# Performance work log

Measured on AMD Instinct MI355X. Metric: run time of the kernel, lower is better.

The kernel has to match this reference:

```python
import jax, jax.numpy as jnp
import numpy as np

B, N, C = 16, 4096, 512
PW, PH = 64, 64  # N = PW * PH
POOL = 2         # attention_pool_scale
D_SCALE = 1.0 / float(np.sqrt(C))


def setup_inputs() -> dict:
    key = jax.random.key(0)
    ks = jax.random.split(key, 4)
    w_std = 1.0 / float(np.sqrt(C))
    return {
        "x": jax.random.normal(ks[0], (B, N, C), dtype=jnp.float32),
        "Wq": jax.random.normal(ks[1], (C, C), dtype=jnp.float32) * w_std,
        "bq": jnp.zeros((C,), dtype=jnp.float32),
        "Wk": jax.random.normal(ks[2], (C, C), dtype=jnp.float32) * w_std,
        "bk": jnp.zeros((C,), dtype=jnp.float32),
        "Wv": jax.random.normal(ks[3], (C, C), dtype=jnp.float32) * w_std,
        "bv": jnp.zeros((C,), dtype=jnp.float32),
    }


def _to_spatial(t):
    # [B, N, C] -> [B, C, PW, PH]
    return t.transpose(0, 2, 1).reshape(t.shape[0], C, PW, PH)


def reference(x, Wq, bq, Wk, bk, Wv, bv):
    # Linear (torch convention y = x @ W^T + b) + sigmoid activation
    def proj(W, b):
        return jax.nn.sigmoid(jnp.einsum('bnc,dc->bnd', x, W) + b)

    Q = _to_spatial(proj(Wq, bq))  # [B, C, PW, PH]
    K = _to_spatial(proj(Wk, bk))
    V = _to_spatial(proj(Wv, bv))

    # avg_pool2d with kernel (POOL, 1): pool over PW axis
    q = Q.reshape(B, C, PW // POOL, POOL, PH).mean(axis=3)  # [B, C, PW/2, PH]
    k = K.reshape(B, C, PW // POOL, POOL, PH).mean(axis=3)

    # Qk = softmax(scale * Q @ k^T): [B, C, PW, PW/2]
    Qk = jax.nn.softmax(D_SCALE * jnp.einsum('bcik,bcjk->bcij', Q, k), axis=-1)
    # Kq = softmax(scale * q @ K^T): [B, C, PW/2, PW]
    Kq = jax.nn.softmax(D_SCALE * jnp.einsum('bcik,bcjk->bcij', q, K), axis=-1)
    # Kqv = Kq @ V: [B, C, PW/2, PH]
    Kqv = jnp.einsum('bcij,bcjk->bcik', Kq, V)
    # out = Qk @ Kqv: [B, C, PW, PH]
    out = jnp.einsum('bcij,bcjk->bcik', Qk, Kqv)

    # spatial -> sequence: [B, C, PW*PH] -> [B, N, C]
    return out.reshape(B, C, N).transpose(0, 2, 1)
```

## Files before the change

### kernel.cpp

```cpp
#include <hip/hip_runtime.h>
#include <hip/hip_bf16.h>
#include <string.h>

typedef __hip_bfloat16  bf16;
typedef __hip_bfloat162 bf162;
typedef __attribute__((ext_vector_type(8))) short short8;
typedef __attribute__((ext_vector_type(4))) float f32x4;

#define NB 16
#define NN 4096
#define NC 512
#define SCALE 0.044194173824159216f
#define LDSTR 56

__global__ __launch_bounds__(256) void cast_x_kernel(
    const float* __restrict__ x, bf16* __restrict__ xb)
{
    size_t i = ((size_t)blockIdx.x * 256 + threadIdx.x) * 8;
    float4 a = *(const float4*)(x + i);
    float4 b = *(const float4*)(x + i + 4);
    bf16 t[8];
    t[0] = __float2bfloat16(a.x); t[1] = __float2bfloat16(a.y);
    t[2] = __float2bfloat16(a.z); t[3] = __float2bfloat16(a.w);
    t[4] = __float2bfloat16(b.x); t[5] = __float2bfloat16(b.y);
    t[6] = __float2bfloat16(b.z); t[7] = __float2bfloat16(b.w);
    uint4 r; memcpy(&r, t, 16);
    *(uint4*)(xb + i) = r;
}

__global__ __launch_bounds__(256) void proj_mfma(
    const bf16* __restrict__ xb,
    const float* __restrict__ Wq, const float* __restrict__ bq,
    const float* __restrict__ Wk, const float* __restrict__ bk,
    const float* __restrict__ Wv, const float* __restrict__ bv,
    bf16* __restrict__ Qs, bf16* __restrict__ Ks, bf16* __restrict__ Vs)
{
    __shared__ __align__(16) char smem[2 * 128 * LDSTR * 2];
    short* As = (short*)smem;
    short* Bs = (short*)(smem + 128 * LDSTR * 2);
    float* st = (float*)smem;

    const int tid = threadIdx.x;
    const int w   = tid >> 6;
    const int l   = tid & 63;
    const int q   = l >> 4;
    const int mrow= l & 15;
    const int wr  = w >> 1;
    const int wc  = w & 1;

    const int bx = blockIdx.x;
    const int m  = bx >> 2;
    const int d0 = (bx & 3) * 128;
    const int r0 = blockIdx.y * 128;
    const int b  = r0 >> 12;
    const int n0 = r0 & 4095;

    const float* W    = (m == 0) ? Wq : (m == 1) ? Wk : Wv;
    const float* bias = (m == 0) ? bq : (m == 1) ? bk : bv;
    bf16*        Out  = (m == 0) ? Qs : (m == 1) ? Ks : Vs;

    f32x4 acc[4][4];
    const f32x4 z = {0.f, 0.f, 0.f, 0.f};
    #pragma unroll
    for (int i = 0; i < 4; ++i)
        #pragma unroll
        for (int j = 0; j < 4; ++j) acc[i][j] = z;

    const int srow0 = tid >> 2;
    const int kseg  = (tid & 3) * 8;

    for (int k0 = 0; k0 < NC; k0 += 32) {
        #pragma unroll
        for (int i = 0; i < 2; ++i) {
            int srow = srow0 + 64 * i;
            uint4 av = *(const uint4*)(xb + (size_t)(r0 + srow) * NC + k0 + kseg);
            *(uint4*)&As[srow * LDSTR + kseg] = av;
        }
        #pragma unroll
        for (int i = 0; i < 2; ++i) {
            int srow = srow0 + 64 * i;
            const float* wp = W + (size_t)(d0 + srow) * NC + k0 + kseg;
            float4 w0 = *(const float4*)(wp);
            float4 w1 = *(const float4*)(wp + 4);
            bf16 t[8];
            t[0] = __float2bfloat16(w0.x); t[1] = __float2bfloat16(w0.y);
            t[2] = __float2bfloat16(w0.z); t[3] = __float2bfloat16(w0.w);
            t[4] = __float2bfloat16(w1.x); t[5] = __float2bfloat16(w1.y);
            t[6] = __float2bfloat16(w1.z); t[7] = __float2bfloat16(w1.w);
            uint4 r; memcpy(&r, t, 16);
            *(uint4*)&Bs[srow * LDSTR + kseg] = r;
        }
        __syncthreads();

        short8 af[4], bfr[4];
        #pragma unroll
        for (int ti = 0; ti < 4; ++ti)
            af[ti] = *(const short8*)&As[(64 * wr + 16 * ti + mrow) * LDSTR + q * 8];
        #pragma unroll
        for (int tj = 0; tj < 4; ++tj)
            bfr[tj] = *(const short8*)&Bs[(64 * wc + 16 * tj + mrow) * LDSTR + q * 8];
        #pragma unroll
        for (int ti = 0; ti < 4; ++ti)
            #pragma unroll
            for (int tj = 0; tj < 4; ++tj)
                acc[ti][tj] = __builtin_amdgcn_mfma_f32_16x16x32_bf16(
                    af[ti], bfr[tj], acc[ti][tj], 0, 0, 0);
        __syncthreads();
    }

    float bb[4];
    #pragma unroll
    for (int tj = 0; tj < 4; ++tj) bb[tj] = bias[d0 + 64 * wc + 16 * tj + mrow];

    #pragma unroll
    for (int dc = 0; dc < 4; ++dc) {
        if (wc == (dc >> 1)) {
            #pragma unroll
            for (int tjh = 0; tjh < 2; ++tjh) {
                int tj = 2 * (dc & 1) + tjh;
                #pragma unroll
                for (int ti = 0; ti < 4; ++ti)
                    #pragma unroll
                    for (int g = 0; g < 4; ++g) {
                        float v  = acc[ti][tj][g] + bb[tj];
                        float sg = 1.0f / (1.0f + __expf(-v));
                        int nl = 64 * wr + 16 * ti + 4 * q + g;
                        int dl = 16 * tjh + mrow;
                        st[nl * 33 + dl] = sg;
                    }
            }
        }
        __syncthreads();
        #pragma unroll
        for (int i = 0; i < 8; ++i) {
            int p     = tid + 256 * i;
            int dl    = p >> 6;
            int npair = tid & 63;
            bf162 v2;
            v2.x = __float2bfloat16(st[(2 * npair    ) * 33 + dl]);
            v2.y = __float2bfloat16(st[(2 * npair + 1) * 33 + dl]);
            size_t d = d0 + 32 * dc + dl;
            ((bf162*)(Out + ((size_t)b * NC + d) * NN + n0))[npair] = v2;
        }
        __syncthreads();
    }
}

__global__ __launch_bounds__(256) void attn_mfma(
    const bf16* __restrict__ Qs, const bf16* __restrict__ Ks,
    const bf16* __restrict__ Vs, bf16* __restrict__ Os)
{
    __shared__ __align__(16) char smem[24064];
    bf16* VT  = (bf16*)smem;
    bf16* S1b = (bf16*)(smem + 9216);
    bf16* S2b = (bf16*)(smem + 9216 + 5120);
    bf16* KVT = (bf16*)(smem + 9216 + 5120 + 4608);

    const int tid = threadIdx.x;
    const int w   = tid >> 6;
    const int l   = tid & 63;
    const int m   = l & 15;
    const int q   = l >> 4;
    const size_t base = (size_t)blockIdx.x * NN;

    {
        const uint4* src = (const uint4*)(Vs + base);
        #pragma unroll
        for (int v = 0; v < 2; ++v) {
            int e = tid + 256 * v;
            uint4 r = src[e];
            bf16 tmp[8]; memcpy(tmp, &r, 16);
            int pw  = e >> 3;
            int ph0 = (e & 7) * 8;
            #pragma unroll
            for (int t = 0; t < 8; ++t)
                VT[(ph0 + t) * 72 + pw] = tmp[t];
        }
    }

    f32x4 tacc[4];
    {
        const f32x4 z = {0.f, 0.f, 0.f, 0.f};
        short8 aQ[2];
        #pragma unroll
        for (int ks = 0; ks < 2; ++ks)
            aQ[ks] = *(const short8*)(Qs + base + (16 * w + m) * 64 + q * 8 + 32 * ks);
        #pragma unroll
        for (int tj = 0; tj < 4; ++tj) {
            tacc[tj] = z;
            #pragma unroll
            for (int ks = 0; ks < 2; ++ks) {
                short8 bK = *(const short8*)(Ks + base + (16 * tj + m) * 64 + q * 8 + 32 * ks);
                tacc[tj] = __builtin_amdgcn_mfma_f32_16x16x32_bf16(aQ[ks], bK, tacc[tj], 0, 0, 0);
            }
        }
    }

    {
        float p[4][4], e[4][4], mx[4], s[4];
        #pragma unroll
        for (int r = 0; r < 4; ++r) mx[r] = -1e30f;
        #pragma unroll
        for (int t = 0; t < 4; ++t)
            #pragma unroll
            for (int r = 0; r < 4; ++r) {
                float v  = tacc[t][r];
                float pv = (v + __shfl_xor(v, 1)) * (0.5f * SCALE);
                p[t][r] = pv;
                mx[r]   = fmaxf(mx[r], pv);
            }
        #pragma unroll
        for (int r = 0; r < 4; ++r) {
            #pragma unroll
            for (int d = 1; d < 16; d <<= 1)
                mx[r] = fmaxf(mx[r], __shfl_xor(mx[r], d));
            s[r] = 0.f;
        }
        #pragma unroll
        for (int t = 0; t < 4; ++t)
            #pragma unroll
            for (int r = 0; r < 4; ++r) {
                e[t][r] = __expf(p[t][r] - mx[r]);
                s[r] += e[t][r];
            }
        #pragma unroll
        for (int r = 0; r < 4; ++r) {
            #pragma unroll
            for (int d = 1; d < 16; d <<= 1)
                s[r] += __shfl_xor(s[r], d);
            s[r] = 2.0f / s[r];
        }
        if (!(l & 1)) {
            int jc = m >> 1;
            #pragma unroll
            for (int t = 0; t < 4; ++t)
                #pragma unroll
                for (int r = 0; r < 4; ++r)
                    S1b[(16 * w + q * 4 + r) * 40 + t * 8 + jc] =
                        __float2bfloat16(e[t][r] * s[r]);
        }
    }

    {
        float p2[4][2], e2[4][2], mx[2], s[2];
        #pragma unroll
        for (int h = 0; h < 2; ++h) mx[h] = -1e30f;
        #pragma unroll
        for (int t = 0; t < 4; ++t)
            #pragma unroll
            for (int h = 0; h < 2; ++h) {
                float pv = (tacc[t][2 * h] + tacc[t][2 * h + 1]) * (0.5f * SCALE);
                p2[t][h] = pv;
                mx[h]    = fmaxf(mx[h], pv);
            }
        #pragma unroll
        for (int h = 0; h < 2; ++h) {
            #pragma unroll
            for (int d = 1; d < 16; d <<= 1)
                mx[h] = fmaxf(mx[h], __shfl_xor(mx[h], d));
            s[h] = 0.f;
        }
        #pragma unroll
        for (int t = 0; t < 4; ++t)
            #pragma unroll
            for (int h = 0; h < 2; ++h) {
                e2[t][h] = __expf(p2[t][h] - mx[h]);
                s[h] += e2[t][h];
            }
        #pragma unroll
        for (int h = 0; h < 2; ++h) {
            #pragma unroll
            for (int d = 1; d < 16; d <<= 1)
                s[h] += __shfl_xor(s[h], d);
            s[h] = 1.0f / s[h];
        }
        #pragma unroll
        for (int t = 0; t < 4; ++t)
            #pragma unroll
            for (int h = 0; h < 2; ++h)
                S2b[(8 * w + q * 2 + h) * 72 + t * 16 + m] =
                    __float2bfloat16(e2[t][h] * s[h]);
    }
    __syncthreads();

    {
        short8 aV[2];
        #pragma unroll
        for (int ks = 0; ks < 2; ++ks)
            aV[ks] = *(const short8*)&VT[(16 * w + m) * 72 + q * 8 + 32 * ks];
        #pragma unroll
        for (int tn = 0; tn < 2; ++tn) {
            f32x4 kacc = {0.f, 0.f, 0.f, 0.f};
            #pragma unroll
            for (int ks = 0; ks < 2; ++ks) {
                short8 bS = *(const short8*)&S2b[(16 * tn + m) * 72 + q * 8 + 32 * ks];
                kacc = __builtin_amdgcn_mfma_f32_16x16x32_bf16(aV[ks], bS, kacc, 0, 0, 0);
            }
            #pragma unroll
            for (int r = 0; r < 4; ++r)
                KVT[(16 * w + q * 4 + r) * 40 + 16 * tn + m] = __float2bfloat16(kacc[r]);
        }
    }
    __syncthreads();

    f32x4 oacc[4];
    {
        short8 aS = *(const short8*)&S1b[(16 * w + m) * 40 + q * 8];
        #pragma unroll
        for (int tn = 0; tn < 4; ++tn) {
            short8 bKV = *(const short8*)&KVT[(16 * tn + m) * 40 + q * 8];
            f32x4 z = {0.f, 0.f, 0.f, 0.f};
            oacc[tn] = __builtin_amdgcn_mfma_f32_16x16x32_bf16(aS, bKV, z, 0, 0, 0);
        }
    }

    {
        bf16* OutS = VT;
        #pragma unroll
        for (int tn = 0; tn < 4; ++tn)
            #pragma unroll
            for (int r = 0; r < 4; ++r)
                OutS[(16 * w + q * 4 + r) * 72 + 16 * tn + m] = __float2bfloat16(oacc[tn][r]);
        __syncthreads();
        uint* Og = (uint*)(Os + base);
        #pragma unroll
        for (int v = 0; v < 8; ++v) {
            int e  = tid + 256 * v;
            int i  = e >> 5;
            int pp = e & 31;
            Og[e] = *(uint*)&OutS[i * 72 + 2 * pp];
        }
    }
}

__global__ __launch_bounds__(256) void unspat_kernel(
    const bf16* __restrict__ Os, float* __restrict__ out)
{
    __shared__ float t[32][65];
    const int b  = blockIdx.z;
    const int c0 = blockIdx.y * 32;
    const int n0 = blockIdx.x * 64;
    const int tx = threadIdx.x & 31;
    const int ty = threadIdx.x >> 5;
    const bf162* src = (const bf162*)(Os + ((size_t)b * NC + c0) * NN + n0);
    #pragma unroll
    for (int r = 0; r < 4; ++r) {
        int cc = ty + r * 8;
        float2 f = __bfloat1622float2(src[(size_t)cc * (NN/2) + tx]);
        t[cc][2*tx] = f.x; t[cc][2*tx+1] = f.y;
    }
    __syncthreads();
    float* dst = out + ((size_t)b * NN + n0) * NC + c0;
    #pragma unroll
    for (int r = 0; r < 8; ++r) {
        int nn = ty + r * 8;
        dst[(size_t)nn * NC + tx] = t[tx][nn];
    }
}

extern "C" void kernel_launch(void* const* d_in, const int* in_sizes, int n_in,
                              void* d_out, int out_size, void* d_ws, size_t ws_size,
                              hipStream_t stream)
{
    const float* x  = (const float*)d_in[0];
    const float* Wq = (const float*)d_in[1];
    const float* bq = (const float*)d_in[2];
    const float* Wk = (const float*)d_in[3];
    const float* bk = (const float*)d_in[4];
    const float* Wv = (const float*)d_in[5];
    const float* bv = (const float*)d_in[6];
    float* out = (float*)d_out;

    const size_t S = (size_t)NB * NC * NN;
    bf16* Qb = (bf16*)d_ws;
    bf16* Kb = Qb + S;
    bf16* Vb = Kb + S;
    bf16* xb = (bf16*)d_out;

    cast_x_kernel<<<dim3((NB * NN * NC) / (256 * 8)), 256, 0, stream>>>(x, xb);
    proj_mfma<<<dim3(12, (NB * NN) / 128), 256, 0, stream>>>(
        xb, Wq, bq, Wk, bk, Wv, bv, Qb, Kb, Vb);
    attn_mfma<<<dim3(NB * NC), 256, 0, stream>>>(Qb, Kb, Vb, Qb);
    unspat_kernel<<<dim3(NN / 64, NC / 32, NB), 256, 0, stream>>>(Qb, out);
}
```

Measured before the change: 579.6 us.

## Pre-cast weights to bf16 and stage GEMM tiles with direct global-to-LDS loads

A new kernel converts Wq, Wk and Wv to bf16 once, into spare space in the output buffer. The projection GEMM then reads bf16 weights instead of converting fp32 on every tile load, which removes redundant conversion work and halves weight traffic. Both operand tiles are now loaded with global_load_lds straight into LDS, bypassing registers, and the K step doubles to 64 with two MFMA sub-steps per tile. The padded LDS stride is dropped in favour of an unpadded 64-element row, which may add LDS bank conflicts on the fragment reads.

Result: faster. 554.1 us (-4.4%).

```diff
diff --git a/kernel.cpp b/kernel.cpp
--- a/kernel.cpp
+++ b/kernel.cpp
@@ -11,7 +11,10 @@
 #define NN 4096
 #define NC 512
 #define SCALE 0.044194173824159216f
-#define LDSTR 56
+
+#define GLL16(gp, lp) __builtin_amdgcn_global_load_lds( \
+    (__attribute__((address_space(1))) void*)(gp),      \
+    (__attribute__((address_space(3))) void*)(lp), 16, 0, 0)
 
 __global__ __launch_bounds__(256) void cast_x_kernel(
     const float* __restrict__ x, bf16* __restrict__ xb)
@@ -28,16 +31,32 @@
     *(uint4*)(xb + i) = r;
 }
 
+__global__ __launch_bounds__(256) void cast_w_kernel(
+    const float* __restrict__ Wq, const float* __restrict__ Wk,
+    const float* __restrict__ Wv, bf16* __restrict__ Wb)
+{
+    const float* W = (blockIdx.y == 0) ? Wq : (blockIdx.y == 1) ? Wk : Wv;
+    size_t i = ((size_t)blockIdx.x * 256 + threadIdx.x) * 8;
+    float4 a = *(const float4*)(W + i);
+    float4 b = *(const float4*)(W + i + 4);
+    bf16 t[8];
+    t[0] = __float2bfloat16(a.x); t[1] = __float2bfloat16(a.y);
+    t[2] = __float2bfloat16(a.z); t[3] = __float2bfloat16(a.w);
+    t[4] = __float2bfloat16(b.x); t[5] = __float2bfloat16(b.y);
+    t[6] = __float2bfloat16(b.z); t[7] = __float2bfloat16(b.w);
+    uint4 r; memcpy(&r, t, 16);
+    *(uint4*)(Wb + (size_t)blockIdx.y * (NC * NC) + i) = r;
+}
+
 __global__ __launch_bounds__(256) void proj_mfma(
-    const bf16* __restrict__ xb,
-    const float* __restrict__ Wq, const float* __restrict__ bq,
-    const float* __restrict__ Wk, const float* __restrict__ bk,
-    const float* __restrict__ Wv, const float* __restrict__ bv,
+    const bf16* __restrict__ xb, const bf16* __restrict__ Wb,
+    const float* __restrict__ bq, const float* __restrict__ bk,
+    const float* __restrict__ bv,
     bf16* __restrict__ Qs, bf16* __restrict__ Ks, bf16* __restrict__ Vs)
 {
-    __shared__ __align__(16) char smem[2 * 128 * LDSTR * 2];
+    __shared__ __align__(16) char smem[32768];
     short* As = (short*)smem;
-    short* Bs = (short*)(smem + 128 * LDSTR * 2);
+    short* Bs = (short*)(smem + 16384);
     float* st = (float*)smem;
 
     const int tid = threadIdx.x;
@@ -55,7 +74,7 @@
     const int b  = r0 >> 12;
     const int n0 = r0 & 4095;
 
-    const float* W    = (m == 0) ? Wq : (m == 1) ? Wk : Wv;
+    const bf16*  W    = Wb + (size_t)m * (NC * NC);
     const float* bias = (m == 0) ? bq : (m == 1) ? bk : bv;
     bf16*        Out  = (m == 0) ? Qs : (m == 1) ? Ks : Vs;
 
@@ -66,45 +85,38 @@
         #pragma unroll
         for (int j = 0; j < 4; ++j) acc[i][j] = z;
 
-    const int srow0 = tid >> 2;
-    const int kseg  = (tid & 3) * 8;
-
-    for (int k0 = 0; k0 < NC; k0 += 32) {
-        #pragma unroll
-        for (int i = 0; i < 2; ++i) {
-            int srow = srow0 + 64 * i;
-            uint4 av = *(const uint4*)(xb + (size_t)(r0 + srow) * NC + k0 + kseg);
-            *(uint4*)&As[srow * LDSTR + kseg] = av;
-        }
-        #pragma unroll
-        for (int i = 0; i < 2; ++i) {
-            int srow = srow0 + 64 * i;
-            const float* wp = W + (size_t)(d0 + srow) * NC + k0 + kseg;
-            float4 w0 = *(const float4*)(wp);
-            float4 w1 = *(const float4*)(wp + 4);
-            bf16 t[8];
-            t[0] = __float2bfloat16(w0.x); t[1] = __float2bfloat16(w0.y);
-            t[2] = __float2bfloat16(w0.z); t[3] = __float2bfloat16(w0.w);
-            t[4] = __float2bfloat16(w1.x); t[5] = __float2bfloat16(w1.y);
-            t[6] = __float2bfloat16(w1.z); t[7] = __float2bfloat16(w1.w);
-            uint4 r; memcpy(&r, t, 16);
-            *(uint4*)&Bs[srow * LDSTR + kseg] = r;
-        }
-        __syncthreads();
-
-        short8 af[4], bfr[4];
-        #pragma unroll
-        for (int ti = 0; ti < 4; ++ti)
-            af[ti] = *(const short8*)&As[(64 * wr + 16 * ti + mrow) * LDSTR + q * 8];
-        #pragma unroll
-        for (int tj = 0; tj < 4; ++tj)
-            bfr[tj] = *(const short8*)&Bs[(64 * wc + 16 * tj + mrow) * LDSTR + q * 8];
-        #pragma unroll
-        for (int ti = 0; ti < 4; ++ti)
+    const int srow = tid >> 3;
+    const int scol = (tid & 7) * 8;
+
+    for (int k0 = 0; k0 < NC; k0 += 64) {
+        #pragma unroll
+        for (int c = 0; c < 4; ++c) {
+            int row = srow + 32 * c;
+            GLL16(xb + (size_t)(r0 + row) * NC + k0 + scol, &As[row * 64 + scol]);
+        }
+        #pragma unroll
+        for (int c = 0; c < 4; ++c) {
+            int row = srow + 32 * c;
+            GLL16(W + (size_t)(d0 + row) * NC + k0 + scol, &Bs[row * 64 + scol]);
+        }
+        __syncthreads();
+
+        #pragma unroll
+        for (int ks = 0; ks < 2; ++ks) {
+            short8 af[4], bfr[4];
+            #pragma unroll
+            for (int ti = 0; ti < 4; ++ti)
+                af[ti] = *(const short8*)&As[(64 * wr + 16 * ti + mrow) * 64 + q * 8 + 32 * ks];
             #pragma unroll
             for (int tj = 0; tj < 4; ++tj)
-                acc[ti][tj] = __builtin_amdgcn_mfma_f32_16x16x32_bf16(
-                    af[ti], bfr[tj], acc[ti][tj], 0, 0, 0);
+                bfr[tj] = *(const short8*)&Bs[(64 * wc + 16 * tj + mrow) * 64 + q * 8 + 32 * ks];
+            #pragma unroll
+            for (int ti = 0; ti < 4; ++ti)
+                #pragma unroll
+                for (int tj = 0; tj < 4; ++tj)
+                    acc[ti][tj] = __builtin_amdgcn_mfma_f32_16x16x32_bf16(
+                        af[ti], bfr[tj], acc[ti][tj], 0, 0, 0);
+        }
         __syncthreads();
     }
 
@@ -376,10 +388,12 @@
     bf16* Kb = Qb + S;
     bf16* Vb = Kb + S;
     bf16* xb = (bf16*)d_out;
+    bf16* Wb = ((bf16*)d_out) + S;
 
     cast_x_kernel<<<dim3((NB * NN * NC) / (256 * 8)), 256, 0, stream>>>(x, xb);
+    cast_w_kernel<<<dim3((NC * NC) / (256 * 8), 3), 256, 0, stream>>>(Wq, Wk, Wv, Wb);
     proj_mfma<<<dim3(12, (NB * NN) / 128), 256, 0, stream>>>(
-        xb, Wq, bq, Wk, bk, Wv, bv, Qb, Kb, Vb);
+        xb, Wb, bq, bk, bv, Qb, Kb, Vb);
     attn_mfma<<<dim3(NB * NC), 256, 0, stream>>>(Qb, Kb, Vb, Qb);
     unspat_kernel<<<dim3(NN / 64, NC / 32, NB), 256, 0, stream>>>(Qb, out);
 }
```
